# Kernel tuning notes

Hardware: AMD Instinct MI355X
Metric: run time of the kernel (lower is better)

Reference implementation:

```python
import jax, jax.numpy as jnp
import numpy as np
import math

H = 8      # n_heads
D = 64     # d_model (per-head dim in this module)
QDIM = 512


def setup_inputs() -> dict:
    key = jax.random.key(0)
    ks = jax.random.split(key, 11)
    B, L = 4, 1024
    s = 1.0 / math.sqrt(QDIM)
    inp = {
        "q": jax.random.normal(ks[0], (B, L, QDIM), jnp.float32),
        "k": jax.random.normal(ks[1], (B, L, QDIM), jnp.float32),
        "v": jax.random.normal(ks[2], (B, L, QDIM), jnp.float32),
        # Linear weights (torch layout: [out, in]); biases init to zeros in original
        "wq": jax.random.normal(ks[3], (H * D, QDIM), jnp.float32) * s,
        "bq": jnp.zeros((H * D,), jnp.float32),
        "wk": jax.random.normal(ks[4], (H * D, QDIM), jnp.float32) * s,
        "bk": jnp.zeros((H * D,), jnp.float32),
        "wv": jax.random.normal(ks[5], (H * D, QDIM), jnp.float32) * s,
        "bv": jnp.zeros((H * D,), jnp.float32),
        "wp": jax.random.normal(ks[6], (D, H * D), jnp.float32) * (1.0 / math.sqrt(H * D)),
        "bp": jnp.zeros((D,), jnp.float32),
    }
    return inp


def reference(q, k, v, wq, bq, wk, bk, wv, bv, wp, bp):
    b = q.shape[0]
    # projections, split into heads: [b, L, H, D] -> [b, H, L, D]
    q_s = (q @ wq.T + bq).reshape(b, -1, H, D).transpose(0, 2, 1, 3)
    k_s = (k @ wk.T + bk).reshape(b, -1, H, D).transpose(0, 2, 1, 3)
    v_s = (v @ wv.T + bv).reshape(b, -1, H, D).transpose(0, 2, 1, 3)
    # NOTE: original scales by sqrt(batch_size), not sqrt(d_k)
    scores = jnp.einsum("bhqd,bhkd->bhqk", q_s, k_s) / math.sqrt(b)
    attn = jax.nn.softmax(scores, axis=-1)
    # context = attn^T @ v  (quirk: output seq length = k_len)
    context = jnp.einsum("bhqk,bhqd->bhkd", attn, v_s)
    context = context.transpose(0, 2, 1, 3).reshape(b, -1, H * D)
    output = context @ wp.T + bp  # dropout is identity at eval
    return (output, attn)
```

## Files before the change

kernel.cpp:

```cpp
#include <hip/hip_runtime.h>

#define QD 512
#define NW (512*512)

typedef __attribute__((ext_vector_type(8))) short bf16x8;
typedef __attribute__((ext_vector_type(4))) float f32x4;

#define MFMA16(a,b,c) __builtin_amdgcn_mfma_f32_16x16x32_bf16((a),(b),(c),0,0,0)

static __device__ __forceinline__ short f2bf(float f) {
  unsigned u = __float_as_uint(f);
  u += 0x7fffu + ((u >> 16) & 1u);
  return (short)(u >> 16);
}
static __device__ __forceinline__ float bf2f(short s) {
  return __uint_as_float(((unsigned)(unsigned short)s) << 16);
}

#define GL2LDS16(g, l)                                                        \
  __builtin_amdgcn_global_load_lds(                                           \
      (const __attribute__((address_space(1))) unsigned int*)(g),             \
      (__attribute__((address_space(3))) unsigned int*)(l), 16, 0, 0)

__global__ __launch_bounds__(256) void k_wconv(
    const float* __restrict__ wq, const float* __restrict__ wk,
    const float* __restrict__ wv, const float* __restrict__ wp,
    short* __restrict__ W, short* __restrict__ WPH) {
  int i = blockIdx.x * 256 + threadIdx.x;
  if (i < NW) {
    float f = wq[i]; short h = f2bf(f);
    W[i] = h; W[NW + i] = f2bf(f - bf2f(h));
  } else if (i < 2 * NW) {
    int j = i - NW;
    float f = wk[j]; short h = f2bf(f);
    W[2 * NW + j] = h; W[3 * NW + j] = f2bf(f - bf2f(h));
  } else if (i < 3 * NW) {
    int j = i - 2 * NW;
    W[4 * NW + j] = f2bf(wv[j]);
  } else {
    int j = i - 3 * NW;
    if (j < 64 * QD) WPH[j] = f2bf(wp[j]);
  }
}

__global__ __launch_bounds__(256) void k_xconv(
    const float* __restrict__ q, const float* __restrict__ k, const float* __restrict__ v,
    short* __restrict__ XqH, short* __restrict__ XqL,
    short* __restrict__ XkH, short* __restrict__ XkL, short* __restrict__ XvH) {
  int i = blockIdx.x * 256 + threadIdx.x;
  int t = i >> 18;
  int j = i & 0x3FFFF;
  const float* src = t == 0 ? q : (t == 1 ? k : v);
  f32x4 x0 = *(const f32x4*)(src + (size_t)j * 8);
  f32x4 x1 = *(const f32x4*)(src + (size_t)j * 8 + 4);
  bf16x8 H, L;
#pragma unroll
  for (int jj = 0; jj < 4; ++jj) {
    short h0 = f2bf(x0[jj]); H[jj] = h0; L[jj] = f2bf(x0[jj] - bf2f(h0));
    short h1 = f2bf(x1[jj]); H[jj + 4] = h1; L[jj + 4] = f2bf(x1[jj] - bf2f(h1));
  }
  if (t == 0)      { *(bf16x8*)(XqH + (size_t)j * 8) = H; *(bf16x8*)(XqL + (size_t)j * 8) = L; }
  else if (t == 1) { *(bf16x8*)(XkH + (size_t)j * 8) = H; *(bf16x8*)(XkL + (size_t)j * 8) = L; }
  else             { *(bf16x8*)(XvH + (size_t)j * 8) = H; }
}

__global__ __launch_bounds__(256) void k_proj(
    const short* __restrict__ XH, const short* __restrict__ XL,
    const short* __restrict__ WH, const short* __restrict__ WL,
    const float* __restrict__ bias,
    short* __restrict__ outH, short* __restrict__ outL,
    short* __restrict__ Vt, int mode) {
  __shared__ short Ah[64 * 32], Al[64 * 32], Bh[64 * 32], Bl[64 * 32];
  const int tid = threadIdx.x;
  const int lane = tid & 63;
  const int col = lane & 15, g = lane >> 4;
  const int w = tid >> 6, wr = w >> 1, wc = w & 1;
  const int h = blockIdx.x;
  const int m0 = blockIdx.y * 64;
  const int srow = tid >> 2;
  const int scol = ((tid & 3) ^ (srow & 3)) * 8;
  const size_t xrow = (size_t)(m0 + srow) * QD + scol;
  const size_t wrow = (size_t)(h * 64 + srow) * QD + scol;

  f32x4 zero = {0.f, 0.f, 0.f, 0.f};
  f32x4 acc[2][2] = {{zero, zero}, {zero, zero}};

  for (int kc = 0; kc < 16; ++kc) {
    const int kb = kc * 32;
    GL2LDS16(XH + xrow + kb, &Ah[tid * 8]);
    GL2LDS16(WH + wrow + kb, &Bh[tid * 8]);
    if (mode == 0) {
      GL2LDS16(XL + xrow + kb, &Al[tid * 8]);
      GL2LDS16(WL + wrow + kb, &Bl[tid * 8]);
    }
    __syncthreads();

    bf16x8 a_h[2], a_l[2], b_h[2], b_l[2];
#pragma unroll
    for (int mt = 0; mt < 2; ++mt) {
      int rowa = wr * 32 + mt * 16 + col;
      int off = rowa * 32 + ((g ^ (rowa & 3)) * 8);
      a_h[mt] = *(const bf16x8*)&Ah[off];
      if (mode == 0) a_l[mt] = *(const bf16x8*)&Al[off];
    }
#pragma unroll
    for (int nt = 0; nt < 2; ++nt) {
      int rowb = wc * 32 + nt * 16 + col;
      int off = rowb * 32 + ((g ^ (rowb & 3)) * 8);
      b_h[nt] = *(const bf16x8*)&Bh[off];
      if (mode == 0) b_l[nt] = *(const bf16x8*)&Bl[off];
    }
#pragma unroll
    for (int mt = 0; mt < 2; ++mt)
#pragma unroll
      for (int nt = 0; nt < 2; ++nt) {
        acc[mt][nt] = MFMA16(a_h[mt], b_h[nt], acc[mt][nt]);
        if (mode == 0) {
          acc[mt][nt] = MFMA16(a_l[mt], b_h[nt], acc[mt][nt]);
          acc[mt][nt] = MFMA16(a_h[mt], b_l[nt], acc[mt][nt]);
        }
      }
    __syncthreads();
  }

#pragma unroll
  for (int nt = 0; nt < 2; ++nt) {
    int d = wc * 32 + nt * 16 + col;
    float bias_v = bias[h * 64 + d];
#pragma unroll
    for (int mt = 0; mt < 2; ++mt)
#pragma unroll
      for (int r = 0; r < 4; ++r) {
        int m = m0 + wr * 32 + mt * 16 + g * 4 + r;
        int b = m >> 10, l = m & 1023;
        float val = acc[mt][nt][r] + bias_v;
        if (mode == 0) {
          size_t idx = (((size_t)b * 8 + h) * 1024 + l) * 64 + d;
          short hh = f2bf(val);
          outH[idx] = hh;
          outL[idx] = f2bf(val - bf2f(hh));
        } else {
          Vt[(((size_t)b * 8 + h) * 64 + d) * 1024 + l] = f2bf(val);
        }
      }
  }
}

__global__ __launch_bounds__(256) void k_attn(
    const short* __restrict__ QsH, const short* __restrict__ QsL,
    const short* __restrict__ KsH, const short* __restrict__ KsL,
    float* __restrict__ attn) {
  const int lane = threadIdx.x & 63, w = threadIdx.x >> 6;
  const int col = lane & 15, g = lane >> 4;
  const int bh = blockIdx.y;
  const int q0 = blockIdx.x * 64 + w * 16;
  const size_t base = (size_t)bh * 1024 * 64;

  size_t qoff = base + (size_t)(q0 + col) * 64 + g * 8;
  bf16x8 qh0 = *(const bf16x8*)(QsH + qoff);
  bf16x8 qh1 = *(const bf16x8*)(QsH + qoff + 32);
  bf16x8 ql0 = *(const bf16x8*)(QsL + qoff);
  bf16x8 ql1 = *(const bf16x8*)(QsL + qoff + 32);

  f32x4 zero = {0.f, 0.f, 0.f, 0.f};
  float sum = 0.f;

  for (int kc = 0; kc < 64; ++kc) {
    size_t koff = base + (size_t)(kc * 16 + col) * 64 + g * 8;
    bf16x8 kh0 = *(const bf16x8*)(KsH + koff);
    bf16x8 kh1 = *(const bf16x8*)(KsH + koff + 32);
    bf16x8 kl0 = *(const bf16x8*)(KsL + koff);
    bf16x8 kl1 = *(const bf16x8*)(KsL + koff + 32);
    f32x4 S = zero;
    S = MFMA16(kh0, qh0, S);
    S = MFMA16(kh1, qh1, S);
    S = MFMA16(kl0, qh0, S);
    S = MFMA16(kl1, qh1, S);
    S = MFMA16(kh0, ql0, S);
    S = MFMA16(kh1, ql1, S);
    sum += __expf(S[0] * 0.5f) + __expf(S[1] * 0.5f) +
           __expf(S[2] * 0.5f) + __expf(S[3] * 0.5f);
  }
  sum += __shfl_xor(sum, 16);
  sum += __shfl_xor(sum, 32);
  float inv = 1.f / sum;

  float* ob = attn + (size_t)bh * 1024 * 1024 + (size_t)(q0 + col) * 1024;
  for (int kc = 0; kc < 64; ++kc) {
    size_t koff = base + (size_t)(kc * 16 + col) * 64 + g * 8;
    bf16x8 kh0 = *(const bf16x8*)(KsH + koff);
    bf16x8 kh1 = *(const bf16x8*)(KsH + koff + 32);
    bf16x8 kl0 = *(const bf16x8*)(KsL + koff);
    bf16x8 kl1 = *(const bf16x8*)(KsL + koff + 32);
    f32x4 S = zero;
    S = MFMA16(kh0, qh0, S);
    S = MFMA16(kh1, qh1, S);
    S = MFMA16(kl0, qh0, S);
    S = MFMA16(kl1, qh1, S);
    S = MFMA16(kh0, ql0, S);
    S = MFMA16(kh1, ql1, S);
    f32x4 o;
#pragma unroll
    for (int r = 0; r < 4; ++r) o[r] = __expf(S[r] * 0.5f) * inv;
    *(f32x4*)(ob + kc * 16 + g * 4) = o;
  }
}

__global__ __launch_bounds__(256) void k_ctx(
    const float* __restrict__ attn, const short* __restrict__ Vt,
    short* __restrict__ ctx) {
  const int lane = threadIdx.x & 63, w = threadIdx.x >> 6;
  const int col = lane & 15, g = lane >> 4;
  const int bh = blockIdx.y;
  const int k0 = blockIdx.x * 64 + w * 16;
  const float* ab = attn + (size_t)bh * 1024 * 1024;
  const short* vb = Vt + (size_t)bh * 64 * 1024;

  f32x4 zero = {0.f, 0.f, 0.f, 0.f};
  f32x4 acc[4] = {zero, zero, zero, zero};

  for (int qc = 0; qc < 32; ++qc) {
    const float* ap = ab + (size_t)(qc * 32 + g * 8) * 1024 + k0 + col;
    bf16x8 af;
#pragma unroll
    for (int j = 0; j < 8; ++j) af[j] = f2bf(ap[(size_t)j * 1024]);
#pragma unroll
    for (int nt = 0; nt < 4; ++nt) {
      bf16x8 bfv = *(const bf16x8*)(vb + (size_t)(nt * 16 + col) * 1024 + qc * 32 + g * 8);
      acc[nt] = MFMA16(af, bfv, acc[nt]);
    }
  }
  int b = bh >> 3, h = bh & 7;
#pragma unroll
  for (int nt = 0; nt < 4; ++nt)
#pragma unroll
    for (int r = 0; r < 4; ++r) {
      int kk = k0 + g * 4 + r;
      ctx[((size_t)(b * 1024 + kk)) * 512 + h * 64 + nt * 16 + col] = f2bf(acc[nt][r]);
    }
}

__global__ __launch_bounds__(256) void k_out(
    const short* __restrict__ ctx, const short* __restrict__ WPH,
    const float* __restrict__ bp, float* __restrict__ out) {
  const int lane = threadIdx.x & 63, w = threadIdx.x >> 6;
  const int col = lane & 15, g = lane >> 4;
  const int m0 = blockIdx.x * 64 + w * 16;

  f32x4 zero = {0.f, 0.f, 0.f, 0.f};
  f32x4 acc[4] = {zero, zero, zero, zero};

  for (int kc = 0; kc < 16; ++kc) {
    bf16x8 a = *(const bf16x8*)(ctx + (size_t)(m0 + col) * 512 + kc * 32 + g * 8);
#pragma unroll
    for (int nt = 0; nt < 4; ++nt) {
      bf16x8 bfr = *(const bf16x8*)(WPH + (size_t)(nt * 16 + col) * 512 + kc * 32 + g * 8);
      acc[nt] = MFMA16(a, bfr, acc[nt]);
    }
  }
#pragma unroll
  for (int nt = 0; nt < 4; ++nt) {
    float bias = bp[nt * 16 + col];
#pragma unroll
    for (int r = 0; r < 4; ++r)
      out[(size_t)(m0 + g * 4 + r) * 64 + nt * 16 + col] = acc[nt][r] + bias;
  }
}

extern "C" void kernel_launch(void* const* d_in, const int* in_sizes, int n_in,
                              void* d_out, int out_size, void* d_ws, size_t ws_size,
                              hipStream_t stream) {
  const float* q  = (const float*)d_in[0];
  const float* k  = (const float*)d_in[1];
  const float* v  = (const float*)d_in[2];
  const float* wq = (const float*)d_in[3];
  const float* bq = (const float*)d_in[4];
  const float* wk = (const float*)d_in[5];
  const float* bk = (const float*)d_in[6];
  const float* wv = (const float*)d_in[7];
  const float* bv = (const float*)d_in[8];
  const float* wp = (const float*)d_in[9];
  const float* bp = (const float*)d_in[10];

  float* out  = (float*)d_out;
  float* attn = out + 262144;

  short* S = (short*)d_ws;
  const size_t E = 2097152;
  short* XqH = S;
  short* XqL = S + E;
  short* XkH = S + 2 * E;
  short* XkL = S + 3 * E;
  short* XvH = S + 4 * E;
  short* QsH = S + 5 * E;
  short* QsL = S + 6 * E;
  short* KsH = S;
  short* KsL = S + E;
  short* Vt  = S + 2 * E;
  short* ctx = S + 3 * E;
  short* W   = S + 7 * E;
  short* WPH = W + 5 * (size_t)NW;

  k_wconv<<<dim3(3200), dim3(256), 0, stream>>>(wq, wk, wv, wp, W, WPH);
  k_xconv<<<dim3(3072), dim3(256), 0, stream>>>(q, k, v, XqH, XqL, XkH, XkL, XvH);
  k_proj <<<dim3(8, 64), dim3(256), 0, stream>>>(XqH, XqL, W, W + NW, bq,
                                                 QsH, QsL, nullptr, 0);
  k_proj <<<dim3(8, 64), dim3(256), 0, stream>>>(XkH, XkL, W + 2 * NW, W + 3 * NW, bk,
                                                 KsH, KsL, nullptr, 0);
  k_proj <<<dim3(8, 64), dim3(256), 0, stream>>>(XvH, XvH, W + 4 * NW, W + 4 * NW, bv,
                                                 nullptr, nullptr, Vt, 1);
  k_attn <<<dim3(16, 32), dim3(256), 0, stream>>>(QsH, QsL, KsH, KsL, attn);
  k_ctx  <<<dim3(16, 32), dim3(256), 0, stream>>>(attn, Vt, ctx);
  k_out  <<<dim3(64), dim3(256), 0, stream>>>(ctx, WPH, bp, out);
}
```

Baseline: 367.6 us.

## Fuse attention probability write with context matmul; compute row sums separately

```diff
diff --git a/kernel.cpp b/kernel.cpp
--- a/kernel.cpp
+++ b/kernel.cpp
@@ -4,6 +4,7 @@
 #define NW (512*512)
 
 typedef __attribute__((ext_vector_type(8))) short bf16x8;
+typedef __attribute__((ext_vector_type(4))) short bf16x4;
 typedef __attribute__((ext_vector_type(4))) float f32x4;
 
 #define MFMA16(a,b,c) __builtin_amdgcn_mfma_f32_16x16x32_bf16((a),(b),(c),0,0,0)
@@ -15,6 +16,9 @@
 }
 static __device__ __forceinline__ float bf2f(short s) {
   return __uint_as_float(((unsigned)(unsigned short)s) << 16);
+}
+static __device__ __forceinline__ unsigned pk2(float a, float b) {
+  return (unsigned)(unsigned short)f2bf(a) | (((unsigned)(unsigned short)f2bf(b)) << 16);
 }
 
 #define GL2LDS16(g, l)                                                        \
@@ -69,8 +73,8 @@
     const short* __restrict__ WH, const short* __restrict__ WL,
     const float* __restrict__ bias,
     short* __restrict__ outH, short* __restrict__ outL,
-    short* __restrict__ Vt, int mode) {
-  __shared__ short Ah[64 * 32], Al[64 * 32], Bh[64 * 32], Bl[64 * 32];
+    short* __restrict__ Vt, int mode, float scale) {
+  __shared__ __align__(16) short Ah[64 * 32], Al[64 * 32], Bh[64 * 32], Bl[64 * 32];
   const int tid = threadIdx.x;
   const int lane = tid & 63;
   const int col = lane & 15, g = lane >> 4;
@@ -133,7 +137,7 @@
       for (int r = 0; r < 4; ++r) {
         int m = m0 + wr * 32 + mt * 16 + g * 4 + r;
         int b = m >> 10, l = m & 1023;
-        float val = acc[mt][nt][r] + bias_v;
+        float val = (acc[mt][nt][r] + bias_v) * scale;
         if (mode == 0) {
           size_t idx = (((size_t)b * 8 + h) * 1024 + l) * 64 + d;
           short hh = f2bf(val);
@@ -146,97 +150,131 @@
   }
 }
 
-__global__ __launch_bounds__(256) void k_attn(
+__global__ __launch_bounds__(256) void k_sums(
+    const short* __restrict__ QsH, const short* __restrict__ KsH,
+    float* __restrict__ invp) {
+  __shared__ __align__(16) short KL[32 * 64];
+  const int tid = threadIdx.x;
+  const int lane = tid & 63, w = tid >> 6;
+  const int col = lane & 15, g = lane >> 4;
+  int wgid = blockIdx.x + gridDim.x * blockIdx.y;
+  int nid = (wgid & 7) * 64 + (wgid >> 3);
+  const int qblk = nid & 15, bh = nid >> 4;
+  const int q0 = qblk * 64 + w * 16;
+  const size_t base = (size_t)bh * 65536;
+
+  const short* qp = QsH + base + (size_t)(q0 + col) * 64 + g * 8;
+  bf16x8 qB0 = *(const bf16x8*)qp;
+  bf16x8 qB1 = *(const bf16x8*)(qp + 32);
+
+  const int srow = tid >> 3, sslot = tid & 7;
+  const short* ksrc = KsH + base + (size_t)srow * 64 + ((sslot ^ (srow & 7)) * 8);
+
+  f32x4 zero = {0.f, 0.f, 0.f, 0.f};
+  float sum = 0.f;
+  for (int kb = 0; kb < 32; ++kb) {
+    GL2LDS16(ksrc + kb * 2048, &KL[tid * 8]);
+    __syncthreads();
+#pragma unroll
+    for (int sub = 0; sub < 2; ++sub) {
+      const short* lb = &KL[(sub * 16 + col) * 64];
+      bf16x8 ka0 = *(const bf16x8*)(lb + ((g ^ (col & 7)) * 8));
+      bf16x8 ka1 = *(const bf16x8*)(lb + (((4 + g) ^ (col & 7)) * 8));
+      f32x4 S = zero;
+      S = MFMA16(ka0, qB0, S);
+      S = MFMA16(ka1, qB1, S);
+      sum += __expf(S[0]) + __expf(S[1]) + __expf(S[2]) + __expf(S[3]);
+    }
+    __syncthreads();
+  }
+  sum += __shfl_xor(sum, 16);
+  sum += __shfl_xor(sum, 32);
+  if (lane < 16) invp[bh * 1024 + q0 + col] = 1.f / sum;
+}
+
+__global__ __launch_bounds__(256) void k_pv(
     const short* __restrict__ QsH, const short* __restrict__ QsL,
     const short* __restrict__ KsH, const short* __restrict__ KsL,
-    float* __restrict__ attn) {
-  const int lane = threadIdx.x & 63, w = threadIdx.x >> 6;
+    const short* __restrict__ Vt, const float* __restrict__ invp,
+    float* __restrict__ attn, short* __restrict__ ctx) {
+  __shared__ __align__(16) short QH[32 * 64], QL[32 * 64];
+  const int tid = threadIdx.x;
+  const int lane = tid & 63, w = tid >> 6;
   const int col = lane & 15, g = lane >> 4;
-  const int bh = blockIdx.y;
-  const int q0 = blockIdx.x * 64 + w * 16;
-  const size_t base = (size_t)bh * 1024 * 64;
-
-  size_t qoff = base + (size_t)(q0 + col) * 64 + g * 8;
-  bf16x8 qh0 = *(const bf16x8*)(QsH + qoff);
-  bf16x8 qh1 = *(const bf16x8*)(QsH + qoff + 32);
-  bf16x8 ql0 = *(const bf16x8*)(QsL + qoff);
-  bf16x8 ql1 = *(const bf16x8*)(QsL + qoff + 32);
+  int wgid = blockIdx.x + gridDim.x * blockIdx.y;
+  int nid = (wgid & 7) * 64 + (wgid >> 3);
+  const int kblk = nid & 15, bh = nid >> 4;
+  const int k0 = kblk * 64 + w * 16;
+  const size_t base = (size_t)bh * 65536;
+
+  const short* kp = KsH + base + (size_t)(k0 + col) * 64 + g * 8;
+  bf16x8 khB0 = *(const bf16x8*)kp;
+  bf16x8 khB1 = *(const bf16x8*)(kp + 32);
+  const short* kpl = KsL + base + (size_t)(k0 + col) * 64 + g * 8;
+  bf16x8 klB0 = *(const bf16x8*)kpl;
+  bf16x8 klB1 = *(const bf16x8*)(kpl + 32);
+
+  const short* vb = Vt + base;
+  float* ab = attn + (size_t)bh * 1024 * 1024;
+  const float* invB = invp + bh * 1024;
+
+  const int srow = tid >> 3, sslot = tid & 7;
+  const size_t qsrc = base + (size_t)srow * 64 + ((sslot ^ (srow & 7)) * 8);
 
   f32x4 zero = {0.f, 0.f, 0.f, 0.f};
-  float sum = 0.f;
-
-  for (int kc = 0; kc < 64; ++kc) {
-    size_t koff = base + (size_t)(kc * 16 + col) * 64 + g * 8;
-    bf16x8 kh0 = *(const bf16x8*)(KsH + koff);
-    bf16x8 kh1 = *(const bf16x8*)(KsH + koff + 32);
-    bf16x8 kl0 = *(const bf16x8*)(KsL + koff);
-    bf16x8 kl1 = *(const bf16x8*)(KsL + koff + 32);
-    f32x4 S = zero;
-    S = MFMA16(kh0, qh0, S);
-    S = MFMA16(kh1, qh1, S);
-    S = MFMA16(kl0, qh0, S);
-    S = MFMA16(kl1, qh1, S);
-    S = MFMA16(kh0, ql0, S);
-    S = MFMA16(kh1, ql1, S);
-    sum += __expf(S[0] * 0.5f) + __expf(S[1] * 0.5f) +
-           __expf(S[2] * 0.5f) + __expf(S[3] * 0.5f);
-  }
-  sum += __shfl_xor(sum, 16);
-  sum += __shfl_xor(sum, 32);
-  float inv = 1.f / sum;
-
-  float* ob = attn + (size_t)bh * 1024 * 1024 + (size_t)(q0 + col) * 1024;
-  for (int kc = 0; kc < 64; ++kc) {
-    size_t koff = base + (size_t)(kc * 16 + col) * 64 + g * 8;
-    bf16x8 kh0 = *(const bf16x8*)(KsH + koff);
-    bf16x8 kh1 = *(const bf16x8*)(KsH + koff + 32);
-    bf16x8 kl0 = *(const bf16x8*)(KsL + koff);
-    bf16x8 kl1 = *(const bf16x8*)(KsL + koff + 32);
-    f32x4 S = zero;
-    S = MFMA16(kh0, qh0, S);
-    S = MFMA16(kh1, qh1, S);
-    S = MFMA16(kl0, qh0, S);
-    S = MFMA16(kl1, qh1, S);
-    S = MFMA16(kh0, ql0, S);
-    S = MFMA16(kh1, ql1, S);
-    f32x4 o;
-#pragma unroll
-    for (int r = 0; r < 4; ++r) o[r] = __expf(S[r] * 0.5f) * inv;
-    *(f32x4*)(ob + kc * 16 + g * 4) = o;
-  }
-}
-
-__global__ __launch_bounds__(256) void k_ctx(
-    const float* __restrict__ attn, const short* __restrict__ Vt,
-    short* __restrict__ ctx) {
-  const int lane = threadIdx.x & 63, w = threadIdx.x >> 6;
-  const int col = lane & 15, g = lane >> 4;
-  const int bh = blockIdx.y;
-  const int k0 = blockIdx.x * 64 + w * 16;
-  const float* ab = attn + (size_t)bh * 1024 * 1024;
-  const short* vb = Vt + (size_t)bh * 64 * 1024;
-
-  f32x4 zero = {0.f, 0.f, 0.f, 0.f};
-  f32x4 acc[4] = {zero, zero, zero, zero};
-
-  for (int qc = 0; qc < 32; ++qc) {
-    const float* ap = ab + (size_t)(qc * 32 + g * 8) * 1024 + k0 + col;
-    bf16x8 af;
-#pragma unroll
-    for (int j = 0; j < 8; ++j) af[j] = f2bf(ap[(size_t)j * 1024]);
-#pragma unroll
-    for (int nt = 0; nt < 4; ++nt) {
-      bf16x8 bfv = *(const bf16x8*)(vb + (size_t)(nt * 16 + col) * 1024 + qc * 32 + g * 8);
-      acc[nt] = MFMA16(af, bfv, acc[nt]);
-    }
-  }
+  f32x4 O[4] = {zero, zero, zero, zero};
+
+  for (int cc = 0; cc < 32; ++cc) {
+    GL2LDS16(QsH + qsrc + cc * 2048, &QH[tid * 8]);
+    GL2LDS16(QsL + qsrc + cc * 2048, &QL[tid * 8]);
+    __syncthreads();
+
+    float p[2][4];
+#pragma unroll
+    for (int t = 0; t < 2; ++t) {
+      const short* lh = &QH[(t * 16 + col) * 64];
+      const short* ll = &QL[(t * 16 + col) * 64];
+      int o0 = (g ^ (col & 7)) * 8, o1 = ((4 + g) ^ (col & 7)) * 8;
+      bf16x8 qh0 = *(const bf16x8*)(lh + o0);
+      bf16x8 qh1 = *(const bf16x8*)(lh + o1);
+      bf16x8 ql0 = *(const bf16x8*)(ll + o0);
+      bf16x8 ql1 = *(const bf16x8*)(ll + o1);
+      f32x4 S = zero;
+      S = MFMA16(qh0, khB0, S);
+      S = MFMA16(qh1, khB1, S);
+      S = MFMA16(ql0, khB0, S);
+      S = MFMA16(ql1, khB1, S);
+      S = MFMA16(qh0, klB0, S);
+      S = MFMA16(qh1, klB1, S);
+      f32x4 iv = *(const f32x4*)(invB + cc * 32 + t * 16 + 4 * g);
+      float* ap = ab + (size_t)(cc * 32 + t * 16 + 4 * g) * 1024 + k0 + col;
+#pragma unroll
+      for (int r = 0; r < 4; ++r) {
+        p[t][r] = __expf(S[r]) * iv[r];
+        ap[(size_t)r * 1024] = p[t][r];
+      }
+    }
+    union { bf16x8 v; unsigned u[4]; } pa;
+    pa.u[0] = pk2(p[0][0], p[0][1]); pa.u[1] = pk2(p[0][2], p[0][3]);
+    pa.u[2] = pk2(p[1][0], p[1][1]); pa.u[3] = pk2(p[1][2], p[1][3]);
+#pragma unroll
+    for (int dt = 0; dt < 4; ++dt) {
+      const short* vr = vb + (size_t)(dt * 16 + col) * 1024 + cc * 32 + 4 * g;
+      union { bf16x8 v; bf16x4 h[2]; } vf;
+      vf.h[0] = *(const bf16x4*)vr;
+      vf.h[1] = *(const bf16x4*)(vr + 16);
+      O[dt] = MFMA16(pa.v, vf.v, O[dt]);
+    }
+    __syncthreads();
+  }
+
   int b = bh >> 3, h = bh & 7;
 #pragma unroll
-  for (int nt = 0; nt < 4; ++nt)
+  for (int dt = 0; dt < 4; ++dt)
 #pragma unroll
     for (int r = 0; r < 4; ++r) {
-      int kk = k0 + g * 4 + r;
-      ctx[((size_t)(b * 1024 + kk)) * 512 + h * 64 + nt * 16 + col] = f2bf(acc[nt][r]);
+      int kk = k0 + 4 * g + r;
+      ctx[((size_t)(b * 1024 + kk)) * 512 + h * 64 + dt * 16 + col] = f2bf(O[dt][r]);
     }
 }
 
@@ -300,16 +338,18 @@
   short* ctx = S + 3 * E;
   short* W   = S + 7 * E;
   short* WPH = W + 5 * (size_t)NW;
+  float* invp = (float*)(WPH + 64 * QD);
 
   k_wconv<<<dim3(3200), dim3(256), 0, stream>>>(wq, wk, wv, wp, W, WPH);
   k_xconv<<<dim3(3072), dim3(256), 0, stream>>>(q, k, v, XqH, XqL, XkH, XkL, XvH);
   k_proj <<<dim3(8, 64), dim3(256), 0, stream>>>(XqH, XqL, W, W + NW, bq,
-                                                 QsH, QsL, nullptr, 0);
+                                                 QsH, QsL, nullptr, 0, 0.5f);
   k_proj <<<dim3(8, 64), dim3(256), 0, stream>>>(XkH, XkL, W + 2 * NW, W + 3 * NW, bk,
-                                                 KsH, KsL, nullptr, 0);
+                                                 KsH, KsL, nullptr, 0, 1.0f);
   k_proj <<<dim3(8, 64), dim3(256), 0, stream>>>(XvH, XvH, W + 4 * NW, W + 4 * NW, bv,
-                                                 nullptr, nullptr, Vt, 1);
-  k_attn <<<dim3(16, 32), dim3(256), 0, stream>>>(QsH, QsL, KsH, KsL, attn);
-  k_ctx  <<<dim3(16, 32), dim3(256), 0, stream>>>(attn, Vt, ctx);
+                                                 nullptr, nullptr, Vt, 1, 1.0f);
+  k_sums <<<dim3(16, 32), dim3(256), 0, stream>>>(QsH, KsH, invp);
+  k_pv   <<<dim3(16, 32), dim3(256), 0, stream>>>(QsH, QsL, KsH, KsL, Vt, invp,
+                                                  attn, ctx);
   k_out  <<<dim3(64), dim3(256), 0, stream>>>(ctx, WPH, bp, out);
 }
```

Result: faster. 305.8 us (-16.8%).
